# Kernel tuning notes

Measured on AMD Instinct MI355X. Metric: run time of the kernel, lower is better.

Reference implementation:

```python
import jax, jax.numpy as jnp
import numpy as np

D_IN = 5
H = 512

def _init_params(key):
    ks = jax.random.split(key, 10)
    s1 = 1.0 / np.sqrt(H)
    u = lambda k, shape: jax.random.uniform(k, shape, jnp.float32, -s1, s1)
    return dict(
        W_ih1=u(ks[0], (4 * H, D_IN)), W_hh1=u(ks[1], (4 * H, H)),
        b_ih1=u(ks[2], (4 * H,)), b_hh1=u(ks[3], (4 * H,)),
        W_ih2=u(ks[4], (4 * H, H)), W_hh2=u(ks[5], (4 * H, H)),
        b_ih2=u(ks[6], (4 * H,)), b_hh2=u(ks[7], (4 * H,)),
        W_lin=u(ks[8], (1, H)), b_lin=u(ks[9], (1,)),
    )

def setup_inputs() -> dict:
    key = jax.random.key(0)
    kx, kp = jax.random.split(key)
    T, B = 512, 128
    inp = {"x": jax.random.normal(kx, (T, B, D_IN), dtype=jnp.float32)}
    inp.update(_init_params(kp))
    return inp

def _lstm_cell(x, h, c, W_ih, W_hh, b_ih, b_hh):
    # gates: [B, 4H], PyTorch gate order i, f, g, o
    gates = x @ W_ih.T + b_ih + h @ W_hh.T + b_hh
    i, f, g, o = jnp.split(gates, 4, axis=-1)
    c_new = jax.nn.sigmoid(f) * c + jax.nn.sigmoid(i) * jnp.tanh(g)
    h_new = jax.nn.sigmoid(o) * jnp.tanh(c_new)
    return h_new, c_new

def reference(x, W_ih1, W_hh1, b_ih1, b_hh1, W_ih2, W_hh2, b_ih2, b_hh2, W_lin, b_lin):
    B = x.shape[1]
    z = jnp.zeros((B, H), dtype=x.dtype)

    def step(carry, x_t):
        h1, c1, h2, c2 = carry
        h1, c1 = _lstm_cell(x_t, h1, c1, W_ih1, W_hh1, b_ih1, b_hh1)
        h2, c2 = _lstm_cell(h1, h2, c2, W_ih2, W_hh2, b_ih2, b_hh2)
        out = h2 @ W_lin.T + b_lin  # [B, 1]
        return (h1, c1, h2, c2), out[:, 0]

    _, ys = jax.lax.scan(step, (z, z, z, z), x)  # ys: [T, B]
    return ys.T  # [B, T] == torch.stack(outputs, 1).squeeze(2)
```

## Files before the change

### kernel.cpp

```cpp
#include <hip/hip_runtime.h>
#include <hip/hip_fp16.h>


#define HDIM   512
#define TSTEPS 512
#define BATCH  128
#define DIN    5
#define NGRP   4
#define MGRP   32
#define NB1    16
#define NB2    32
#define RING   16

#define OFF_W1 0u
#define OFF_W2 2097152u
#define OFF_H1 6291456u
#define OFF_H2 8388608u
#define OFF_F1 8650752u
#define OFF_F2 8675328u
#define WS_END 8699904u

typedef _Float16 half8 __attribute__((ext_vector_type(8)));
typedef float    floatx4 __attribute__((ext_vector_type(4)));
typedef unsigned long long u64;

__device__ __forceinline__ float sigf(float v) { return 1.0f / (1.0f + __expf(-v)); }

__device__ __forceinline__ half8 as_h8(uint4 u) {
  union { uint4 u; half8 h; } c; c.u = u; return c.h;
}
__device__ __forceinline__ void ring_st8(_Float16* p, u64 v) {
  __hip_atomic_store((u64*)p, v, __ATOMIC_RELAXED, __HIP_MEMORY_SCOPE_AGENT);
}
__device__ __forceinline__ void lda16(const _Float16* p, uint4* a) {
  asm volatile(
      "global_load_dwordx4 %0, %16, off sc0 sc1\n\t"
      "global_load_dwordx4 %1, %16, off offset:64 sc0 sc1\n\t"
      "global_load_dwordx4 %2, %16, off offset:128 sc0 sc1\n\t"
      "global_load_dwordx4 %3, %16, off offset:192 sc0 sc1\n\t"
      "global_load_dwordx4 %4, %16, off offset:256 sc0 sc1\n\t"
      "global_load_dwordx4 %5, %16, off offset:320 sc0 sc1\n\t"
      "global_load_dwordx4 %6, %16, off offset:384 sc0 sc1\n\t"
      "global_load_dwordx4 %7, %16, off offset:448 sc0 sc1\n\t"
      "global_load_dwordx4 %8, %16, off offset:512 sc0 sc1\n\t"
      "global_load_dwordx4 %9, %16, off offset:576 sc0 sc1\n\t"
      "global_load_dwordx4 %10, %16, off offset:640 sc0 sc1\n\t"
      "global_load_dwordx4 %11, %16, off offset:704 sc0 sc1\n\t"
      "global_load_dwordx4 %12, %16, off offset:768 sc0 sc1\n\t"
      "global_load_dwordx4 %13, %16, off offset:832 sc0 sc1\n\t"
      "global_load_dwordx4 %14, %16, off offset:896 sc0 sc1\n\t"
      "global_load_dwordx4 %15, %16, off offset:960 sc0 sc1\n\t"
      "s_waitcnt vmcnt(0)"
      : "=v"(a[0]), "=v"(a[1]), "=v"(a[2]), "=v"(a[3]),
        "=v"(a[4]), "=v"(a[5]), "=v"(a[6]), "=v"(a[7]),
        "=v"(a[8]), "=v"(a[9]), "=v"(a[10]), "=v"(a[11]),
        "=v"(a[12]), "=v"(a[13]), "=v"(a[14]), "=v"(a[15])
      : "v"(p)
      : "memory");
}
__device__ __forceinline__ void poll_line(const unsigned* line, int n, unsigned tgt,
                                          int lane) {
  for (;;) {
    unsigned v = tgt;
    if (lane < n)
      v = __hip_atomic_load(line + lane, __ATOMIC_RELAXED, __HIP_MEMORY_SCOPE_AGENT);
    if (__all((int)(v >= tgt))) break;
  }
  __asm__ __volatile__("" ::: "memory");
}

extern "C" __global__ void init_kernel(char* __restrict__ ws, float* __restrict__ out,
                                       const float* __restrict__ blin) {
  unsigned tid = blockIdx.x * 256u + threadIdx.x;
  unsigned nz = (WS_END - OFF_H1) / 16u;
  if (tid < nz) ((uint4*)(ws + OFF_H1))[tid] = make_uint4(0, 0, 0, 0);
  if (tid < (unsigned)(BATCH * TSTEPS)) out[tid] = blin[0];
}

extern "C" __global__ void pack_kernel(const float* __restrict__ Whh1,
                                       const float* __restrict__ Wih2,
                                       const float* __restrict__ Whh2,
                                       char* __restrict__ ws) {
  unsigned tid = blockIdx.x * 256u + threadIdx.x;
  const float* src;
  char* dst;
  if (tid < 131072u) {
    unsigned lane = tid & 63u, ks = (tid >> 6) & 15u, gg = (tid >> 10) & 3u,
             h = (tid >> 12) & 1u, j = tid >> 13;
    unsigned cg = j * 32u + h * 16u + (lane & 15u);
    unsigned row = gg * 512u + cg;
    unsigned k0 = ks * 32u + (lane >> 4) * 8u;
    src = Whh1 + (size_t)row * 512u + k0;
    dst = ws + OFF_W1 + (size_t)tid * 16u;
  } else {
    unsigned t2 = tid - 131072u;
    if (t2 >= 262144u) return;
    unsigned lane = t2 & 63u, ksl = (t2 >> 6) & 15u, gg = (t2 >> 10) & 3u,
             kh = (t2 >> 12) & 1u, j = t2 >> 13;
    unsigned cg = j * 16u + (lane & 15u);
    unsigned row = gg * 512u + cg;
    unsigned kp = kh * 512u + ksl * 32u + (lane >> 4) * 8u;
    src = (kp < 512u) ? (Wih2 + (size_t)row * 512u + kp)
                      : (Whh2 + (size_t)row * 512u + (kp - 512u));
    dst = ws + OFF_W2 + (size_t)t2 * 16u;
  }
  float4 lo = ((const float4*)src)[0];
  float4 hi = ((const float4*)src)[1];
  _Float16 v[8] = {(_Float16)lo.x, (_Float16)lo.y, (_Float16)lo.z, (_Float16)lo.w,
                   (_Float16)hi.x, (_Float16)hi.y, (_Float16)hi.z, (_Float16)hi.w};
  *(uint4*)dst = *(const uint4*)v;
}

extern "C" __global__ __launch_bounds__(256, 1) void lstm_persist(
    const float* __restrict__ x,
    const float* __restrict__ Wih1,
    const float* __restrict__ bih1, const float* __restrict__ bhh1,
    const float* __restrict__ bih2, const float* __restrict__ bhh2,
    const float* __restrict__ Wlin,
    float* __restrict__ out,
    char* __restrict__ ws) {
  __shared__ char smem[16384];

  const int blk = blockIdx.x;
  const int xcd = blk & 7;
  const int slot = blk >> 3;
  const int tid = threadIdx.x;
  const int wave = tid >> 6;
  const int lane = tid & 63;
  const int nlane = lane & 15;
  const int quad = lane >> 4;

  _Float16* h1ring = (_Float16*)(ws + OFF_H1);
  _Float16* h2ring = (_Float16*)(ws + OFF_H2);

  if (xcd >= NGRP) {
    const int g = xcd - NGRP;
    const int j = slot;
    if (j >= NB1) return;
    const char* gW = ws + OFF_W1 + (size_t)j * 131072u;

    unsigned* f1g = (unsigned*)(ws + OFF_F1) + (size_t)g * 48 * 32;
    unsigned* f2g = (unsigned*)(ws + OFF_F2) + (size_t)g * 48 * 32;
    const unsigned* myline1 = f1g + (size_t)j * 32;
    const unsigned* mybp    = f2g + (size_t)(32 + j) * 32;
    _Float16* ring = h1ring + (size_t)g * (RING * MGRP * HDIM);
    _Float16* tile = (_Float16*)smem;

    const int mt = wave >> 1;
    const int hh = wave & 1;
    const int cg = j * 32 + hh * 16 + nlane;

    half8 breg[64];
#pragma unroll
    for (int r = 0; r < 64; ++r)
      breg[r] = *(const half8*)(gW + (size_t)((hh * 64 + r) * 64 + lane) * 16);

    float bias_r[4], wih[4][5];
    for (int gg = 0; gg < 4; ++gg) {
      int row = gg * 512 + cg;
      bias_r[gg] = bih1[row] + bhh1[row];
      for (int k = 0; k < 5; ++k) wih[gg][k] = Wih1[row * 5 + k];
    }
    float cstate[4] = {};

    for (int t = 0; t < TSTEPS; ++t) {
      if (t) poll_line(myline1, NB1, (unsigned)t, lane);
      if ((t & 7) == 0 && t >= 16) poll_line(mybp, NB2, (unsigned)(t - 8), lane);

      const _Float16* ap =
          ring + (size_t)((t + RING - 1) & (RING - 1)) * (MGRP * HDIM) +
          mt * 16 * HDIM + nlane * HDIM + quad * 8;
      uint4 areg[16];
      lda16(ap, areg);

      float xr[4][5];
#pragma unroll
      for (int r = 0; r < 4; ++r) {
        int b = g * MGRP + mt * 16 + quad * 4 + r;
        const float* xp = x + ((size_t)t * BATCH + b) * DIN;
#pragma unroll
        for (int k = 0; k < 5; ++k) xr[r][k] = xp[k];
      }
      floatx4 acc[4];
#pragma unroll
      for (int gg = 0; gg < 4; ++gg) {
#pragma unroll
        for (int r = 0; r < 4; ++r) {
          float s = bias_r[gg];
#pragma unroll
          for (int k = 0; k < 5; ++k) s += xr[r][k] * wih[gg][k];
          acc[gg][r] = s;
        }
      }
#pragma unroll
      for (int ks = 0; ks < 16; ++ks) {
        half8 av = as_h8(areg[ks]);
#pragma unroll
        for (int gg = 0; gg < 4; ++gg)
          acc[gg] = __builtin_amdgcn_mfma_f32_16x16x32_f16(av, breg[gg * 16 + ks],
                                                           acc[gg], 0, 0, 0);
      }
#pragma unroll
      for (int r = 0; r < 4; ++r) {
        float iv = acc[0][r], fv = acc[1][r], gv = acc[2][r], ov = acc[3][r];
        float cn = sigf(fv) * cstate[r] + sigf(iv) * tanhf(gv);
        float hn = sigf(ov) * tanhf(cn);
        cstate[r] = cn;
        tile[(mt * 16 + quad * 4 + r) * 32 + hh * 16 + nlane] = (_Float16)hn;
      }
      __syncthreads();
      {
        _Float16* hout = ring + (size_t)(t & (RING - 1)) * (MGRP * HDIM);
        u64 v = *(const u64*)(tile + (tid >> 3) * 32 + (tid & 7) * 4);
        ring_st8(hout + (tid >> 3) * HDIM + j * 32 + (tid & 7) * 4, v);
      }
      __syncthreads();
      if (tid < 48)
        __hip_atomic_fetch_add(f1g + (size_t)tid * 32 + j, 1u, __ATOMIC_RELAXED,
                               __HIP_MEMORY_SCOPE_AGENT);
    }
  } else {
    const int g = xcd;
    const int j = slot;
    const char* gW = ws + OFF_W2 + (size_t)j * 131072u;

    unsigned* f1g = (unsigned*)(ws + OFF_F1) + (size_t)g * 48 * 32;
    unsigned* f2g = (unsigned*)(ws + OFF_F2) + (size_t)g * 48 * 32;
    const unsigned* myline1 = f1g + (size_t)(16 + j) * 32;
    const unsigned* myline2 = f2g + (size_t)j * 32;
    const _Float16* h1rd = h1ring + (size_t)g * (RING * MGRP * HDIM);
    _Float16* ring2 = h2ring + (size_t)g * (2 * MGRP * HDIM);
    floatx4* pbase = (floatx4*)smem;
    _Float16* tile2 = (_Float16*)(smem + 8192);

    const int kh = wave & 1;
    const int mt = wave >> 1;
    const int cg = j * 16 + nlane;

    half8 breg[64];
#pragma unroll
    for (int r = 0; r < 64; ++r)
      breg[r] = *(const half8*)(gW + (size_t)((kh * 64 + r) * 64 + lane) * 16);

    float bias_r[4];
    for (int gg = 0; gg < 4; ++gg) {
      int row = gg * 512 + cg;
      bias_r[gg] = bih2[row] + bhh2[row];
    }
    const float wl = Wlin[cg];
    float cstate[4] = {};

    for (int t = 0; t < TSTEPS; ++t) {
      if (kh == 0) poll_line(myline1, NB1, (unsigned)(t + 1), lane);
      else if (t)  poll_line(myline2, NB2, (unsigned)t, lane);

      const _Float16* abase = (kh == 0)
          ? h1rd + (size_t)(t & (RING - 1)) * (MGRP * HDIM) + mt * 16 * HDIM +
                nlane * HDIM + quad * 8
          : ring2 + (size_t)((t + 1) & 1) * (MGRP * HDIM) + mt * 16 * HDIM +
                nlane * HDIM + quad * 8;
      uint4 areg[16];
      lda16(abase, areg);

      floatx4 acc[4];
#pragma unroll
      for (int gg = 0; gg < 4; ++gg)
        acc[gg] = (kh == 0)
            ? (floatx4){bias_r[gg], bias_r[gg], bias_r[gg], bias_r[gg]}
            : (floatx4){0.f, 0.f, 0.f, 0.f};
#pragma unroll
      for (int ks = 0; ks < 16; ++ks) {
        half8 av = as_h8(areg[ks]);
#pragma unroll
        for (int gg = 0; gg < 4; ++gg)
          acc[gg] = __builtin_amdgcn_mfma_f32_16x16x32_f16(av, breg[gg * 16 + ks],
                                                           acc[gg], 0, 0, 0);
      }
      if (kh == 1) {
#pragma unroll
        for (int gg = 0; gg < 4; ++gg) pbase[(mt * 4 + gg) * 64 + lane] = acc[gg];
      }
      __syncthreads();
      float red[4];
      if (kh == 0) {
#pragma unroll
        for (int gg = 0; gg < 4; ++gg) acc[gg] += pbase[(mt * 4 + gg) * 64 + lane];
#pragma unroll
        for (int r = 0; r < 4; ++r) {
          float iv = acc[0][r], fv = acc[1][r], gv = acc[2][r], ov = acc[3][r];
          float cn = sigf(fv) * cstate[r] + sigf(iv) * tanhf(gv);
          float hn = sigf(ov) * tanhf(cn);
          cstate[r] = cn;
          tile2[(mt * 16 + quad * 4 + r) * 16 + nlane] = (_Float16)hn;
          red[r] = wl * hn;
        }
      }
      __syncthreads();
      if (tid < 128) {
        u64 v = *(const u64*)(tile2 + (tid >> 2) * 16 + (tid & 3) * 4);
        ring_st8(ring2 + (size_t)(t & 1) * (MGRP * HDIM) + (tid >> 2) * HDIM +
                     j * 16 + (tid & 3) * 4, v);
      }
      __syncthreads();
      if (tid < 48)
        __hip_atomic_fetch_add(f2g + (size_t)tid * 32 + j, 1u, __ATOMIC_RELAXED,
                               __HIP_MEMORY_SCOPE_AGENT);
      if (kh == 0) {
#pragma unroll
        for (int r = 0; r < 4; ++r) {
          float v2 = red[r];
          v2 += __shfl_xor(v2, 1, 64);
          v2 += __shfl_xor(v2, 2, 64);
          v2 += __shfl_xor(v2, 4, 64);
          v2 += __shfl_xor(v2, 8, 64);
          red[r] = v2;
        }
        if (nlane == 0) {
#pragma unroll
          for (int r = 0; r < 4; ++r) {
            int b = g * MGRP + mt * 16 + quad * 4 + r;
            atomicAdd(out + (size_t)b * TSTEPS + t, red[r]);
          }
        }
      }
    }
  }
}

extern "C" void kernel_launch(void* const* d_in, const int* in_sizes, int n_in,
                              void* d_out, int out_size, void* d_ws, size_t ws_size,
                              hipStream_t stream) {
  const float* x    = (const float*)d_in[0];
  const float* Wih1 = (const float*)d_in[1];
  const float* Whh1 = (const float*)d_in[2];
  const float* bih1 = (const float*)d_in[3];
  const float* bhh1 = (const float*)d_in[4];
  const float* Wih2 = (const float*)d_in[5];
  const float* Whh2 = (const float*)d_in[6];
  const float* bih2 = (const float*)d_in[7];
  const float* bhh2 = (const float*)d_in[8];
  const float* Wlin = (const float*)d_in[9];
  const float* blin = (const float*)d_in[10];
  float* out = (float*)d_out;
  char* ws = (char*)d_ws;

  init_kernel<<<640, 256, 0, stream>>>(ws, out, blin);
  pack_kernel<<<1536, 256, 0, stream>>>(Whh1, Wih2, Whh2, ws);
  lstm_persist<<<256, 256, 0, stream>>>(x, Wih1, bih1, bhh1, bih2, bhh2, Wlin, out, ws);
}
```

Baseline: 2.318 ms.

## Restructure layer-2 blocks with dedicated poller waves and LDS-held input weights

Layer-2 blocks previously split K across wave pairs and reduced partial sums through LDS with several __syncthreads per step. Now waves 0-1 each compute a full 16-row tile. They take the W_ih2 half from LDS and the W_hh2 half from registers. Waves 2-3 become dedicated pollers of the global h1/h2 flags and forward progress through LDS counters, and block barriers are replaced by per-wave LDS atomics. Poll loops gain an iteration cap, which risks silently proceeding on stale data if a wait exceeds the cap, and half the waves no longer do compute.

```diff
diff --git a/kernel.cpp b/kernel.cpp
--- a/kernel.cpp
+++ b/kernel.cpp
@@ -11,6 +11,7 @@
 #define NB1    16
 #define NB2    32
 #define RING   16
+#define SPIN_CAP 16384
 
 #define OFF_W1 0u
 #define OFF_W2 2097152u
@@ -31,6 +32,33 @@
 }
 __device__ __forceinline__ void ring_st8(_Float16* p, u64 v) {
   __hip_atomic_store((u64*)p, v, __ATOMIC_RELAXED, __HIP_MEMORY_SCOPE_AGENT);
+}
+__device__ __forceinline__ void flag_add(unsigned* p) {
+  __hip_atomic_fetch_add(p, 1u, __ATOMIC_RELAXED, __HIP_MEMORY_SCOPE_AGENT);
+}
+__device__ __forceinline__ void poll_line(const unsigned* line, int n, unsigned tgt,
+                                          int lane) {
+  for (int it = 0; it < SPIN_CAP; ++it) {
+    unsigned v = tgt;
+    if (lane < n)
+      v = __hip_atomic_load(line + lane, __ATOMIC_RELAXED, __HIP_MEMORY_SCOPE_AGENT);
+    if (__all((int)(v >= tgt))) break;
+  }
+  __asm__ __volatile__("" ::: "memory");
+}
+__device__ __forceinline__ unsigned lds_add(unsigned* p) {
+  return __hip_atomic_fetch_add(p, 1u, __ATOMIC_RELAXED, __HIP_MEMORY_SCOPE_WORKGROUP);
+}
+__device__ __forceinline__ unsigned lds_ld(const unsigned* p) {
+  return __hip_atomic_load(p, __ATOMIC_RELAXED, __HIP_MEMORY_SCOPE_WORKGROUP);
+}
+__device__ __forceinline__ void lds_st(unsigned* p, unsigned v) {
+  __hip_atomic_store(p, v, __ATOMIC_RELAXED, __HIP_MEMORY_SCOPE_WORKGROUP);
+}
+__device__ __forceinline__ void lds_spin(const unsigned* p, unsigned tgt) {
+  for (int it = 0; it < SPIN_CAP; ++it)
+    if (lds_ld(p) >= tgt) break;
+  __asm__ __volatile__("" ::: "memory");
 }
 __device__ __forceinline__ void lda16(const _Float16* p, uint4* a) {
   asm volatile(
@@ -51,22 +79,12 @@
       "global_load_dwordx4 %14, %16, off offset:896 sc0 sc1\n\t"
       "global_load_dwordx4 %15, %16, off offset:960 sc0 sc1\n\t"
       "s_waitcnt vmcnt(0)"
-      : "=v"(a[0]), "=v"(a[1]), "=v"(a[2]), "=v"(a[3]),
-        "=v"(a[4]), "=v"(a[5]), "=v"(a[6]), "=v"(a[7]),
-        "=v"(a[8]), "=v"(a[9]), "=v"(a[10]), "=v"(a[11]),
-        "=v"(a[12]), "=v"(a[13]), "=v"(a[14]), "=v"(a[15])
+      : "=&v"(a[0]), "=&v"(a[1]), "=&v"(a[2]), "=&v"(a[3]),
+        "=&v"(a[4]), "=&v"(a[5]), "=&v"(a[6]), "=&v"(a[7]),
+        "=&v"(a[8]), "=&v"(a[9]), "=&v"(a[10]), "=&v"(a[11]),
+        "=&v"(a[12]), "=&v"(a[13]), "=&v"(a[14]), "=&v"(a[15])
       : "v"(p)
       : "memory");
-}
-__device__ __forceinline__ void poll_line(const unsigned* line, int n, unsigned tgt,
-                                          int lane) {
-  for (;;) {
-    unsigned v = tgt;
-    if (lane < n)
-      v = __hip_atomic_load(line + lane, __ATOMIC_RELAXED, __HIP_MEMORY_SCOPE_AGENT);
-    if (__all((int)(v >= tgt))) break;
-  }
-  __asm__ __volatile__("" ::: "memory");
 }
 
 extern "C" __global__ void init_kernel(char* __restrict__ ws, float* __restrict__ out,
@@ -119,7 +137,8 @@
     const float* __restrict__ Wlin,
     float* __restrict__ out,
     char* __restrict__ ws) {
-  __shared__ char smem[16384];
+  __shared__ char smem[66624];
+  unsigned* cnt = (unsigned*)(smem + 66560);
 
   const int blk = blockIdx.x;
   const int xcd = blk & 7;
@@ -216,8 +235,7 @@
       }
       __syncthreads();
       if (tid < 48)
-        __hip_atomic_fetch_add(f1g + (size_t)tid * 32 + j, 1u, __ATOMIC_RELAXED,
-                               __HIP_MEMORY_SCOPE_AGENT);
+        flag_add(f1g + (size_t)tid * 32 + j);
     }
   } else {
     const int g = xcd;
@@ -226,21 +244,44 @@
 
     unsigned* f1g = (unsigned*)(ws + OFF_F1) + (size_t)g * 48 * 32;
     unsigned* f2g = (unsigned*)(ws + OFF_F2) + (size_t)g * 48 * 32;
-    const unsigned* myline1 = f1g + (size_t)(16 + j) * 32;
-    const unsigned* myline2 = f2g + (size_t)j * 32;
+    const unsigned* l_h1 = f1g + (size_t)(16 + j) * 32;
+    const unsigned* l_h2 = f2g + (size_t)j * 32;
     const _Float16* h1rd = h1ring + (size_t)g * (RING * MGRP * HDIM);
     _Float16* ring2 = h2ring + (size_t)g * (2 * MGRP * HDIM);
-    floatx4* pbase = (floatx4*)smem;
-    _Float16* tile2 = (_Float16*)(smem + 8192);
-
-    const int kh = wave & 1;
-    const int mt = wave >> 1;
+    const half8* wlds = (const half8*)smem;
+    _Float16* tile2 = (_Float16*)(smem + 65536);
+
+    {
+      const uint4* src = (const uint4*)gW;
+      uint4* dst = (uint4*)smem;
+#pragma unroll
+      for (int i = 0; i < 16; ++i) dst[tid + i * 256] = src[tid + i * 256];
+    }
+    if (tid < 16) cnt[tid] = 0;
+    __syncthreads();
+
+    if (wave == 2) {
+      for (unsigned s = 1; s < TSTEPS; ++s) {
+        poll_line(l_h2, NB2, s, lane);
+        if (lane == 0) lds_st(cnt + 1, s);
+      }
+      return;
+    }
+    if (wave == 3) {
+      for (unsigned s = 1; s <= TSTEPS; ++s) {
+        poll_line(l_h1, NB1, s, lane);
+        if (lane == 0) lds_st(cnt + 2, s);
+      }
+      return;
+    }
+
+    const int mt = wave;
     const int cg = j * 16 + nlane;
 
     half8 breg[64];
 #pragma unroll
     for (int r = 0; r < 64; ++r)
-      breg[r] = *(const half8*)(gW + (size_t)((kh * 64 + r) * 64 + lane) * 16);
+      breg[r] = *(const half8*)(gW + 65536u + (size_t)(r * 64 + lane) * 16);
 
     float bias_r[4];
     for (int gg = 0; gg < 4; ++gg) {
@@ -251,23 +292,28 @@
     float cstate[4] = {};
 
     for (int t = 0; t < TSTEPS; ++t) {
-      if (kh == 0) poll_line(myline1, NB1, (unsigned)(t + 1), lane);
-      else if (t)  poll_line(myline2, NB2, (unsigned)t, lane);
-
-      const _Float16* abase = (kh == 0)
-          ? h1rd + (size_t)(t & (RING - 1)) * (MGRP * HDIM) + mt * 16 * HDIM +
-                nlane * HDIM + quad * 8
-          : ring2 + (size_t)((t + 1) & 1) * (MGRP * HDIM) + mt * 16 * HDIM +
-                nlane * HDIM + quad * 8;
+      lds_spin(cnt + 2, (unsigned)(t + 1));
+      const _Float16* ap1 = h1rd + (size_t)(t & (RING - 1)) * (MGRP * HDIM) +
+                            mt * 16 * HDIM + nlane * HDIM + quad * 8;
       uint4 areg[16];
-      lda16(abase, areg);
+      lda16(ap1, areg);
 
       floatx4 acc[4];
 #pragma unroll
       for (int gg = 0; gg < 4; ++gg)
-        acc[gg] = (kh == 0)
-            ? (floatx4){bias_r[gg], bias_r[gg], bias_r[gg], bias_r[gg]}
-            : (floatx4){0.f, 0.f, 0.f, 0.f};
+        acc[gg] = (floatx4){bias_r[gg], bias_r[gg], bias_r[gg], bias_r[gg]};
+#pragma unroll
+      for (int ks = 0; ks < 16; ++ks) {
+        half8 av = as_h8(areg[ks]);
+#pragma unroll
+        for (int gg = 0; gg < 4; ++gg)
+          acc[gg] = __builtin_amdgcn_mfma_f32_16x16x32_f16(
+              av, wlds[(size_t)(gg * 16 + ks) * 64 + lane], acc[gg], 0, 0, 0);
+      }
+      if (t) lds_spin(cnt + 1, (unsigned)t);
+      const _Float16* ap2 = ring2 + (size_t)((t + 1) & 1) * (MGRP * HDIM) +
+                            mt * 16 * HDIM + nlane * HDIM + quad * 8;
+      lda16(ap2, areg);
 #pragma unroll
       for (int ks = 0; ks < 16; ++ks) {
         half8 av = as_h8(areg[ks]);
@@ -276,51 +322,43 @@
           acc[gg] = __builtin_amdgcn_mfma_f32_16x16x32_f16(av, breg[gg * 16 + ks],
                                                            acc[gg], 0, 0, 0);
       }
-      if (kh == 1) {
-#pragma unroll
-        for (int gg = 0; gg < 4; ++gg) pbase[(mt * 4 + gg) * 64 + lane] = acc[gg];
-      }
-      __syncthreads();
       float red[4];
-      if (kh == 0) {
-#pragma unroll
-        for (int gg = 0; gg < 4; ++gg) acc[gg] += pbase[(mt * 4 + gg) * 64 + lane];
+#pragma unroll
+      for (int r = 0; r < 4; ++r) {
+        float iv = acc[0][r], fv = acc[1][r], gv = acc[2][r], ov = acc[3][r];
+        float cn = sigf(fv) * cstate[r] + sigf(iv) * tanhf(gv);
+        float hn = sigf(ov) * tanhf(cn);
+        cstate[r] = cn;
+        tile2[(mt * 16 + quad * 4 + r) * 16 + nlane] = (_Float16)hn;
+        red[r] = wl * hn;
+      }
+      {
+        int rl = lane >> 2, c4 = (lane & 3) * 4;
+        asm volatile("s_waitcnt lgkmcnt(0)" ::: "memory");
+        u64 v = *(const u64*)(tile2 + (mt * 16 + rl) * 16 + c4);
+        ring_st8(ring2 + (size_t)(t & 1) * (MGRP * HDIM) +
+                     (size_t)(mt * 16 + rl) * HDIM + j * 16 + c4, v);
+      }
+      asm volatile("s_waitcnt vmcnt(0)" ::: "memory");
+      unsigned old = 0;
+      if (lane == 0) old = lds_add(cnt);
+      old = __shfl(old, 0, 64);
+      if ((int)old == 2 * t + 1 && lane < 48)
+        flag_add(f2g + (size_t)lane * 32 + j);
+#pragma unroll
+      for (int r = 0; r < 4; ++r) {
+        float v2 = red[r];
+        v2 += __shfl_xor(v2, 1, 64);
+        v2 += __shfl_xor(v2, 2, 64);
+        v2 += __shfl_xor(v2, 4, 64);
+        v2 += __shfl_xor(v2, 8, 64);
+        red[r] = v2;
+      }
+      if (nlane == 0) {
 #pragma unroll
         for (int r = 0; r < 4; ++r) {
-          float iv = acc[0][r], fv = acc[1][r], gv = acc[2][r], ov = acc[3][r];
-          float cn = sigf(fv) * cstate[r] + sigf(iv) * tanhf(gv);
-          float hn = sigf(ov) * tanhf(cn);
-          cstate[r] = cn;
-          tile2[(mt * 16 + quad * 4 + r) * 16 + nlane] = (_Float16)hn;
-          red[r] = wl * hn;
-        }
-      }
-      __syncthreads();
-      if (tid < 128) {
-        u64 v = *(const u64*)(tile2 + (tid >> 2) * 16 + (tid & 3) * 4);
-        ring_st8(ring2 + (size_t)(t & 1) * (MGRP * HDIM) + (tid >> 2) * HDIM +
-                     j * 16 + (tid & 3) * 4, v);
-      }
-      __syncthreads();
-      if (tid < 48)
-        __hip_atomic_fetch_add(f2g + (size_t)tid * 32 + j, 1u, __ATOMIC_RELAXED,
-                               __HIP_MEMORY_SCOPE_AGENT);
-      if (kh == 0) {
-#pragma unroll
-        for (int r = 0; r < 4; ++r) {
-          float v2 = red[r];
-          v2 += __shfl_xor(v2, 1, 64);
-          v2 += __shfl_xor(v2, 2, 64);
-          v2 += __shfl_xor(v2, 4, 64);
-          v2 += __shfl_xor(v2, 8, 64);
-          red[r] = v2;
-        }
-        if (nlane == 0) {
-#pragma unroll
-          for (int r = 0; r < 4; ++r) {
-            int b = g * MGRP + mt * 16 + quad * 4 + r;
-            atomicAdd(out + (size_t)b * TSTEPS + t, red[r]);
-          }
+          int b = g * MGRP + mt * 16 + quad * 4 + r;
+          atomicAdd(out + (size_t)b * TSTEPS + t, red[r]);
         }
       }
     }
```

Result: slower. 3.002 ms (+29.5%).
